# Kernel tuning notes

Measured on AMD Instinct MI355X. Metric: run time of the kernel, lower is better.

Reference implementation:

```python
import jax, jax.numpy as jnp
import numpy as np

B = 256        # number of trees
L0 = 4096      # leaves per tree
L1 = 256       # layer-1 nodes per tree
D = 128        # input_dim == hidden_dim
OUT = 32       # output classes
EPS = 1e-5
N0 = B * L0    # 1,048,576 total leaves
N1 = B * L1    # 65,536 layer-1 nodes
N2 = B         # one root per tree


def _bn(x, g, b):
    # training-mode BatchNorm1d: biased variance over the node axis
    m = jnp.mean(x, axis=0)
    v = jnp.mean((x - m) ** 2, axis=0)
    return g * (x - m) * jax.lax.rsqrt(v + EPS) + b


def _mlp(h, w1, b1, g, beta, w2, b2):
    # GIN-style 2-layer MLP: relu(bn(linear)) -> linear
    return jax.nn.relu(_bn(h @ w1 + b1, g, beta)) @ w2 + b2


def setup_inputs() -> dict:
    key = jax.random.key(0)
    ks = jax.random.split(key, 16)

    def lin(k, fin, fout):
        kw, kb = jax.random.split(k)
        s = 1.0 / np.sqrt(fin)
        return (jax.random.uniform(kw, (fin, fout), jnp.float32, -s, s),
                jax.random.uniform(kb, (fout,), jnp.float32, -s, s))

    x = jax.random.normal(ks[0], (N0, D), jnp.float32)
    # structured tree indices: contiguous children per parent, contiguous trees
    parent1 = jnp.arange(N0, dtype=jnp.int64) // (L0 // L1)   # leaf -> layer1 parent (global)
    parent2 = jnp.arange(N1, dtype=jnp.int64) // L1           # layer1 -> root (global)
    tree0 = jnp.arange(N0, dtype=jnp.int64) // L0             # leaf -> tree id
    tree1 = jnp.arange(N1, dtype=jnp.int64) // L1             # layer1 node -> tree id

    m1w1, m1b1 = lin(ks[1], D, D)
    m1w2, m1b2 = lin(ks[2], D, D)
    m2w1, m2b1 = lin(ks[3], D, D)
    m2w2, m2b2 = lin(ks[4], D, D)
    wp, bp = lin(ks[5], D + 2 * D, OUT)

    ones = jnp.ones((D,), jnp.float32)
    zeros = jnp.zeros((D,), jnp.float32)
    return {
        "x": x, "parent1": parent1, "parent2": parent2, "tree0": tree0, "tree1": tree1,
        "mlp1_w1": m1w1, "mlp1_b1": m1b1, "mlp1_g": ones, "mlp1_beta": zeros,
        "mlp1_w2": m1w2, "mlp1_b2": m1b2, "bn1_g": ones, "bn1_b": zeros,
        "mlp2_w1": m2w1, "mlp2_b1": m2b1, "mlp2_g": ones, "mlp2_beta": zeros,
        "mlp2_w2": m2w2, "mlp2_b2": m2b2, "bn2_g": ones, "bn2_b": zeros,
        "wp": wp, "bp": bp,
    }


def reference(x, parent1, parent2, tree0, tree1,
              mlp1_w1, mlp1_b1, mlp1_g, mlp1_beta, mlp1_w2, mlp1_b2, bn1_g, bn1_b,
              mlp2_w1, mlp2_b1, mlp2_g, mlp2_beta, mlp2_w2, mlp2_b2, bn2_g, bn2_b,
              wp, bp):
    # layer 1: sparse child-sum (spmm with all-ones tree adjacency == segment_sum)
    p1 = jax.ops.segment_sum(x, parent1, num_segments=N1)              # [N1, D]
    h1 = jax.nn.relu(_bn(_mlp(p1, mlp1_w1, mlp1_b1, mlp1_g, mlp1_beta, mlp1_w2, mlp1_b2), bn1_g, bn1_b))
    # layer 2 (roots)
    p2 = jax.ops.segment_sum(h1, parent2, num_segments=N2)             # [B, D]
    h2 = jax.nn.relu(_bn(_mlp(p2, mlp2_w1, mlp2_b1, mlp2_g, mlp2_beta, mlp2_w2, mlp2_b2), bn2_g, bn2_b))
    # tree sum-pooling of layers 0..depth-1; layer depth is already per-tree
    g0 = jax.ops.segment_sum(x, tree0, num_segments=B)                 # [B, D]
    g1 = jax.ops.segment_sum(h1, tree1, num_segments=B)                # [B, D]
    rep = jnp.concatenate([g0, g1, h2], axis=1)                        # [B, 3D]
    return jax.nn.softmax(rep @ wp + bp, axis=1)                       # [B, OUT]
```

## Files before the change

### kernel.cpp

```cpp
#include <hip/hip_runtime.h>
#include <math.h>

#define D      128
#define D4     32
#define NTREE  256
#define NL1    65536
#define EPSBN  1e-5f

#define SC_OFF 0L
#define SD_OFF 256L
#define G0_OFF 512L
#define P2_OFF 33280L
#define ZERO_CNT 66048
#define SA_OFF 66048L
#define SB_OFF 66304L
#define T2_OFF 66560L
#define PBA_OFF 99328L
#define PBB_OFF 361472L
#define T1_OFF 623616L
#define U_OFF  4817920L

#define FMA4(A_, S_, W_) { (A_).x = fmaf((S_),(W_).x,(A_).x); (A_).y = fmaf((S_),(W_).y,(A_).y); \
                           (A_).z = fmaf((S_),(W_).z,(A_).z); (A_).w = fmaf((S_),(W_).w,(A_).w); }
#define ADD4(A_, B_)     { (A_).x += (B_).x; (A_).y += (B_).y; (A_).z += (B_).z; (A_).w += (B_).w; }
#define SQ4(Q_, V_)      { (Q_).x = fmaf((V_).x,(V_).x,(Q_).x); (Q_).y = fmaf((V_).y,(V_).y,(Q_).y); \
                           (Q_).z = fmaf((V_).z,(V_).z,(Q_).z); (Q_).w = fmaf((V_).w,(V_).w,(Q_).w); }
#define F4Z              make_float4(0.f,0.f,0.f,0.f)

__device__ __forceinline__ unsigned short f2b(float f) {
    unsigned u = __float_as_uint(f);
    return (unsigned short)((u + 0x7FFFu + ((u >> 16) & 1u)) >> 16);
}
__device__ __forceinline__ float b2f(unsigned short h) {
    return __uint_as_float(((unsigned)h) << 16);
}

__global__ __launch_bounds__(256) void k_zero(float* __restrict__ ws) {
    int i = blockIdx.x * 256 + threadIdx.x;
    if (i < ZERO_CNT) ws[i] = 0.f;
}

__global__ __launch_bounds__(256) void k_fused1(const float* __restrict__ x,
        const float* __restrict__ w1, const float* __restrict__ b1,
        unsigned short* __restrict__ t1, float* __restrict__ g0,
        float* __restrict__ pbufA)
{
    __shared__ __align__(16) float tile[64][D];
    __shared__ __align__(16) float red[2][8][D];
    const int t = threadIdx.x, b = blockIdx.x;
    const int w  = t >> 6;
    const int ln = t & 63;
    const int lc = ln & 31;
    const float4* __restrict__ x4 = (const float4*)x;

    float4 gacc = F4Z;
    #pragma unroll
    for (int pp = 0; pp < 4; ++pp) {
        const int p0 = pp * 16 + w * 4;
        #pragma unroll
        for (int r = 0; r < 4; ++r) {
            const long prow = (long)b * 64 + p0 + r;
            const long base = prow * 512 + ln;
            float4 a = F4Z;
            #pragma unroll
            for (int j = 0; j < 8; ++j) {
                float4 v = x4[base + j * 64];
                ADD4(a, v)
            }
            float4 o;
            o.x = __shfl_xor(a.x, 32); o.y = __shfl_xor(a.y, 32);
            o.z = __shfl_xor(a.z, 32); o.w = __shfl_xor(a.w, 32);
            ADD4(a, o)
            if (ln < 32) {
                *(float4*)&tile[p0 + r][lc*4] = a;
                ADD4(gacc, a)
            }
        }
    }
    if (ln < 32) *(float4*)&red[0][w][lc*4] = gacc;
    __syncthreads();
    if (t < 32) {
        float4 G = F4Z;
        #pragma unroll
        for (int g = 0; g < 4; ++g) { float4 vg = *(const float4*)&red[0][g][t*4]; ADD4(G, vg) }
        const int tree = b >> 2;
        atomicAdd(&g0[tree*D + t*4+0], G.x); atomicAdd(&g0[tree*D + t*4+1], G.y);
        atomicAdd(&g0[tree*D + t*4+2], G.z); atomicAdd(&g0[tree*D + t*4+3], G.w);
    }

    const int tc = t & 31, rg = t >> 5;
    ushort4* __restrict__ tv = (ushort4*)t1;
    const long base = (long)b * 64;
    float4 acc[8];
    const float4 bb = ((const float4*)b1)[tc];
    #pragma unroll
    for (int r = 0; r < 8; ++r) acc[r] = bb;
    const float4* __restrict__ wv = (const float4*)w1;
    #pragma unroll 4
    for (int k4 = 0; k4 < 32; ++k4) {
        float4 wr0 = wv[(k4*4+0)*D4 + tc];
        float4 wr1 = wv[(k4*4+1)*D4 + tc];
        float4 wr2 = wv[(k4*4+2)*D4 + tc];
        float4 wr3 = wv[(k4*4+3)*D4 + tc];
        #pragma unroll
        for (int r = 0; r < 8; ++r) {
            float4 a4 = *(const float4*)&tile[rg*8 + r][k4*4];
            FMA4(acc[r], a4.x, wr0) FMA4(acc[r], a4.y, wr1)
            FMA4(acc[r], a4.z, wr2) FMA4(acc[r], a4.w, wr3)
        }
    }
    #pragma unroll
    for (int r = 0; r < 8; ++r) {
        ushort4 h;
        h.x = f2b(acc[r].x); h.y = f2b(acc[r].y);
        h.z = f2b(acc[r].z); h.w = f2b(acc[r].w);
        tv[(base + rg*8 + r) * D4 + tc] = h;
    }

    float4 s4 = F4Z, q4 = F4Z;
    #pragma unroll
    for (int r = 0; r < 8; ++r) { ADD4(s4, acc[r]) SQ4(q4, acc[r]) }
    __syncthreads();
    *(float4*)&red[0][rg][tc*4] = s4;
    *(float4*)&red[1][rg][tc*4] = q4;
    __syncthreads();
    if (t < 32) {
        float4 S = F4Z;
        #pragma unroll
        for (int g = 0; g < 8; ++g) { float4 vs = *(const float4*)&red[0][g][t*4]; ADD4(S, vs) }
        *(float4*)&pbufA[b*256 + t*4] = S;
    } else if (t < 64) {
        const int c = t - 32;
        float4 Q = F4Z;
        #pragma unroll
        for (int g = 0; g < 8; ++g) { float4 vq = *(const float4*)&red[1][g][c*4]; ADD4(Q, vq) }
        *(float4*)&pbufA[b*256 + 128 + c*4] = Q;
    }
}

__global__ __launch_bounds__(256) void k_statR(const float* __restrict__ pbuf,
                                               float* __restrict__ stats)
{
    __shared__ float red[8][32];
    const int t = threadIdx.x, b = blockIdx.x;
    const int c = b * 32 + (t & 31);
    const int g = t >> 5;
    float s = 0.f;
    #pragma unroll 8
    for (int r = g; r < 1024; r += 8) s += pbuf[r*256 + c];
    red[g][t & 31] = s;
    __syncthreads();
    if (t < 32) {
        float S = 0.f;
        #pragma unroll
        for (int gg = 0; gg < 8; ++gg) S += red[gg][t];
        stats[b*32 + t] = S;
    }
}

__global__ __launch_bounds__(256) void k_mm2(const unsigned short* __restrict__ t1,
        const float* __restrict__ w2, const float* __restrict__ b2,
        const float* __restrict__ mg, const float* __restrict__ mbe,
        const float* __restrict__ statsA, unsigned short* __restrict__ u,
        float* __restrict__ pbufB)
{
    __shared__ __align__(16) float tile[64][D];
    __shared__ __align__(16) float red[2][8][D];
    const int t = threadIdx.x, b = blockIdx.x;
    const int tc = t & 31, rg = t >> 5;
    const ushort4* __restrict__ tv = (const ushort4*)t1;
    ushort4* __restrict__ uv = (ushort4*)u;
    const long base = (long)b * 64;

    float4 scv, shv;
    {
        const float inv = 1.f / (float)NL1;
        #pragma unroll
        for (int i = 0; i < 4; ++i) {
            const int c = tc*4 + i;
            float m  = statsA[c] * inv;
            float vv = statsA[D + c] * inv - m * m;
            float rs = rsqrtf(vv + EPSBN);
            float sc = mg[c] * rs;
            ((float*)&scv)[i] = sc;
            ((float*)&shv)[i] = mbe[c] - m * sc;
        }
    }
    #pragma unroll
    for (int i = 0; i < 8; ++i) {
        const int row = i * 8 + rg;
        ushort4 hv = tv[(base + row) * D4 + tc];
        float4 v = make_float4(b2f(hv.x), b2f(hv.y), b2f(hv.z), b2f(hv.w));
        float4 y;
        y.x = fmaxf(fmaf(v.x, scv.x, shv.x), 0.f);
        y.y = fmaxf(fmaf(v.y, scv.y, shv.y), 0.f);
        y.z = fmaxf(fmaf(v.z, scv.z, shv.z), 0.f);
        y.w = fmaxf(fmaf(v.w, scv.w, shv.w), 0.f);
        *(float4*)&tile[row][tc*4] = y;
    }
    __syncthreads();

    float4 acc[8];
    const float4 bb = ((const float4*)b2)[tc];
    #pragma unroll
    for (int r = 0; r < 8; ++r) acc[r] = bb;
    const float4* __restrict__ wv = (const float4*)w2;
    #pragma unroll 4
    for (int k4 = 0; k4 < 32; ++k4) {
        float4 wr0 = wv[(k4*4+0)*D4 + tc];
        float4 wr1 = wv[(k4*4+1)*D4 + tc];
        float4 wr2 = wv[(k4*4+2)*D4 + tc];
        float4 wr3 = wv[(k4*4+3)*D4 + tc];
        #pragma unroll
        for (int r = 0; r < 8; ++r) {
            float4 a4 = *(const float4*)&tile[rg*8 + r][k4*4];
            FMA4(acc[r], a4.x, wr0) FMA4(acc[r], a4.y, wr1)
            FMA4(acc[r], a4.z, wr2) FMA4(acc[r], a4.w, wr3)
        }
    }
    #pragma unroll
    for (int r = 0; r < 8; ++r) {
        ushort4 h;
        h.x = f2b(acc[r].x); h.y = f2b(acc[r].y);
        h.z = f2b(acc[r].z); h.w = f2b(acc[r].w);
        uv[(base + rg*8 + r) * D4 + tc] = h;
    }

    float4 s4 = F4Z, q4 = F4Z;
    #pragma unroll
    for (int r = 0; r < 8; ++r) { ADD4(s4, acc[r]) SQ4(q4, acc[r]) }
    __syncthreads();
    *(float4*)&red[0][rg][tc*4] = s4;
    *(float4*)&red[1][rg][tc*4] = q4;
    __syncthreads();
    if (t < 32) {
        float4 S = F4Z;
        #pragma unroll
        for (int g = 0; g < 8; ++g) { float4 vs = *(const float4*)&red[0][g][t*4]; ADD4(S, vs) }
        *(float4*)&pbufB[b*256 + t*4] = S;
    } else if (t < 64) {
        const int c = t - 32;
        float4 Q = F4Z;
        #pragma unroll
        for (int g = 0; g < 8; ++g) { float4 vq = *(const float4*)&red[1][g][c*4]; ADD4(Q, vq) }
        *(float4*)&pbufB[b*256 + 128 + c*4] = Q;
    }
}

__global__ __launch_bounds__(256) void k_pool(const unsigned short* __restrict__ u,
        const float* __restrict__ bg, const float* __restrict__ bb_,
        const float* __restrict__ statsB, float* __restrict__ p2)
{
    __shared__ __align__(16) float red[8][D];
    const int t = threadIdx.x, b = blockIdx.x;
    const int tree = b >> 3, chunk = b & 7;
    const int tc = t & 31, rr = t >> 5;
    const ushort4* __restrict__ uv = (const ushort4*)u;

    float4 scv, shv;
    {
        const float inv = 1.f / (float)NL1;
        #pragma unroll
        for (int i = 0; i < 4; ++i) {
            const int c = tc*4 + i;
            float m  = statsB[c] * inv;
            float vv = statsB[D + c] * inv - m * m;
            float rs = rsqrtf(vv + EPSBN);
            float sc = bg[c] * rs;
            ((float*)&scv)[i] = sc;
            ((float*)&shv)[i] = bb_[c] - m * sc;
        }
    }
    const long rbase = (long)tree * 256 + chunk * 32;
    float4 ps = F4Z;
    #pragma unroll
    for (int i = 0; i < 4; ++i) {
        const int row = i * 8 + rr;
        ushort4 hv = uv[(rbase + row) * D4 + tc];
        float4 v = make_float4(b2f(hv.x), b2f(hv.y), b2f(hv.z), b2f(hv.w));
        ps.x += fmaxf(fmaf(v.x, scv.x, shv.x), 0.f);
        ps.y += fmaxf(fmaf(v.y, scv.y, shv.y), 0.f);
        ps.z += fmaxf(fmaf(v.z, scv.z, shv.z), 0.f);
        ps.w += fmaxf(fmaf(v.w, scv.w, shv.w), 0.f);
    }
    *(float4*)&red[rr][tc*4] = ps;
    __syncthreads();
    if (t < 32) {
        float4 S = F4Z;
        #pragma unroll
        for (int g = 0; g < 8; ++g) { float4 vs = *(const float4*)&red[g][t*4]; ADD4(S, vs) }
        atomicAdd(&p2[tree*D + t*4+0], S.x); atomicAdd(&p2[tree*D + t*4+1], S.y);
        atomicAdd(&p2[tree*D + t*4+2], S.z); atomicAdd(&p2[tree*D + t*4+3], S.w);
    }
}

__global__ __launch_bounds__(256) void k_root1(const float* __restrict__ p2,
        const float* __restrict__ w1, const float* __restrict__ b1,
        float* __restrict__ t2, float* __restrict__ statsC)
{
    __shared__ __align__(16) float ps[8][D];
    __shared__ __align__(16) float red[2][8][D];
    const int t = threadIdx.x, b = blockIdx.x;
    const int j4 = t & 31, rr = t >> 5;
    *(float4*)&ps[rr][j4*4] = ((const float4*)p2)[(b*8 + rr)*D4 + j4];
    __syncthreads();
    const int row = t >> 5, tc = t & 31;
    const float4* wv = (const float4*)w1;
    float4 acc = ((const float4*)b1)[tc];
    #pragma unroll 8
    for (int k4 = 0; k4 < 32; ++k4) {
        float4 a = *(const float4*)&ps[row][k4*4];
        float4 wr0 = wv[(k4*4+0)*D4 + tc];
        float4 wr1 = wv[(k4*4+1)*D4 + tc];
        float4 wr2 = wv[(k4*4+2)*D4 + tc];
        float4 wr3 = wv[(k4*4+3)*D4 + tc];
        FMA4(acc, a.x, wr0) FMA4(acc, a.y, wr1) FMA4(acc, a.z, wr2) FMA4(acc, a.w, wr3)
    }
    ((float4*)t2)[(b*8 + row)*D4 + tc] = acc;
    float4 q;
    q.x = acc.x*acc.x; q.y = acc.y*acc.y; q.z = acc.z*acc.z; q.w = acc.w*acc.w;
    *(float4*)&red[0][row][tc*4] = acc;
    *(float4*)&red[1][row][tc*4] = q;
    __syncthreads();
    if (t < D) {
        float S = 0.f, Q = 0.f;
        #pragma unroll
        for (int g = 0; g < 8; ++g) { S += red[0][g][t]; Q += red[1][g][t]; }
        atomicAdd(&statsC[t], S);
        atomicAdd(&statsC[D+t], Q);
    }
}

__global__ __launch_bounds__(256) void k_root2(float* __restrict__ t2,
        const float* __restrict__ mg, const float* __restrict__ mb,
        const float* __restrict__ statsC,
        const float* __restrict__ w2, const float* __restrict__ b2,
        float* __restrict__ statsD)
{
    __shared__ __align__(16) float ysr[8][D];
    __shared__ __align__(16) float red[2][8][D];
    __shared__ __align__(16) float scs[D], shs[D];
    const int t = threadIdx.x, b = blockIdx.x;
    if (t < D) {
        float m = statsC[t] * (1.f / 256.f);
        float v = statsC[D+t] * (1.f / 256.f) - m * m;
        float rs = rsqrtf(v + EPSBN);
        float sc = mg[t] * rs;
        scs[t] = sc;
        shs[t] = mb[t] - m * sc;
    }
    __syncthreads();
    const int j4 = t & 31, rr = t >> 5;
    {
        float4 uu = ((const float4*)t2)[(b*8 + rr)*D4 + j4];
        float4 sc4 = *(const float4*)&scs[j4*4];
        float4 sh4 = *(const float4*)&shs[j4*4];
        float4 y;
        y.x = fmaxf(fmaf(uu.x, sc4.x, sh4.x), 0.f);
        y.y = fmaxf(fmaf(uu.y, sc4.y, sh4.y), 0.f);
        y.z = fmaxf(fmaf(uu.z, sc4.z, sh4.z), 0.f);
        y.w = fmaxf(fmaf(uu.w, sc4.w, sh4.w), 0.f);
        *(float4*)&ysr[rr][j4*4] = y;
    }
    __syncthreads();
    const int row = t >> 5, tc = t & 31;
    const float4* wv = (const float4*)w2;
    float4 acc = ((const float4*)b2)[tc];
    #pragma unroll 8
    for (int k4 = 0; k4 < 32; ++k4) {
        float4 a = *(const float4*)&ysr[row][k4*4];
        float4 wr0 = wv[(k4*4+0)*D4 + tc];
        float4 wr1 = wv[(k4*4+1)*D4 + tc];
        float4 wr2 = wv[(k4*4+2)*D4 + tc];
        float4 wr3 = wv[(k4*4+3)*D4 + tc];
        FMA4(acc, a.x, wr0) FMA4(acc, a.y, wr1) FMA4(acc, a.z, wr2) FMA4(acc, a.w, wr3)
    }
    ((float4*)t2)[(b*8 + row)*D4 + tc] = acc;
    float4 q;
    q.x = acc.x*acc.x; q.y = acc.y*acc.y; q.z = acc.z*acc.z; q.w = acc.w*acc.w;
    *(float4*)&red[0][row][tc*4] = acc;
    *(float4*)&red[1][row][tc*4] = q;
    __syncthreads();
    if (t < D) {
        float S = 0.f, Q = 0.f;
        #pragma unroll
        for (int g = 0; g < 8; ++g) { S += red[0][g][t]; Q += red[1][g][t]; }
        atomicAdd(&statsD[t], S);
        atomicAdd(&statsD[D+t], Q);
    }
}

__global__ __launch_bounds__(128) void k_final(const float* __restrict__ u2,
        const float* __restrict__ statsD,
        const float* __restrict__ bg, const float* __restrict__ bb_,
        const float* __restrict__ g0, const float* __restrict__ p2,
        const float* __restrict__ wp, const float* __restrict__ bp,
        float* __restrict__ out)
{
    __shared__ __align__(16) float reps[3*D];
    const int t = threadIdx.x, tree = blockIdx.x;
    if (t < D) {
        float m = statsD[t] * (1.f / 256.f);
        float v = statsD[D+t] * (1.f / 256.f) - m * m;
        float rs = rsqrtf(v + EPSBN);
        float sc = bg[t] * rs;
        float sh = bb_[t] - m * sc;
        reps[2*D + t] = fmaxf(fmaf(u2[tree*D + t], sc, sh), 0.f);
        reps[t]       = g0[tree*D + t];
        reps[D + t]   = p2[tree*D + t];
    }
    __syncthreads();
    if (t < 32) {
        float acc = bp[t];
        #pragma unroll 8
        for (int j = 0; j < 3*D; ++j) acc = fmaf(reps[j], wp[j*32 + t], acc);
        float mx = acc;
        #pragma unroll
        for (int mk = 16; mk > 0; mk >>= 1) mx = fmaxf(mx, __shfl_xor(mx, mk));
        float e = expf(acc - mx);
        float s = e;
        #pragma unroll
        for (int mk = 16; mk > 0; mk >>= 1) s += __shfl_xor(s, mk);
        out[tree*32 + t] = e / s;
    }
}

extern "C" void kernel_launch(void* const* d_in, const int* in_sizes, int n_in,
                              void* d_out, int out_size, void* d_ws, size_t ws_size,
                              hipStream_t stream)
{
    const float* x    = (const float*)d_in[0];
    const float* m1w1 = (const float*)d_in[5];
    const float* m1b1 = (const float*)d_in[6];
    const float* m1g  = (const float*)d_in[7];
    const float* m1be = (const float*)d_in[8];
    const float* m1w2 = (const float*)d_in[9];
    const float* m1b2 = (const float*)d_in[10];
    const float* bn1g = (const float*)d_in[11];
    const float* bn1b = (const float*)d_in[12];
    const float* m2w1 = (const float*)d_in[13];
    const float* m2b1 = (const float*)d_in[14];
    const float* m2g  = (const float*)d_in[15];
    const float* m2be = (const float*)d_in[16];
    const float* m2w2 = (const float*)d_in[17];
    const float* m2b2 = (const float*)d_in[18];
    const float* bn2g = (const float*)d_in[19];
    const float* bn2b = (const float*)d_in[20];
    const float* wp   = (const float*)d_in[21];
    const float* bp   = (const float*)d_in[22];
    float* out = (float*)d_out;
    float* ws  = (float*)d_ws;

    float* sC  = ws + SC_OFF;
    float* sD  = ws + SD_OFF;
    float* g0  = ws + G0_OFF;
    float* p2  = ws + P2_OFF;
    float* sA  = ws + SA_OFF;
    float* sB  = ws + SB_OFF;
    float* t2  = ws + T2_OFF;
    float* pbA = ws + PBA_OFF;
    float* pbB = ws + PBB_OFF;
    unsigned short* t1 = (unsigned short*)(ws + T1_OFF);
    unsigned short* u  = (unsigned short*)(ws + U_OFF);

    hipLaunchKernelGGL(k_zero,   dim3(258),  dim3(256), 0, stream, ws);
    hipLaunchKernelGGL(k_fused1, dim3(1024), dim3(256), 0, stream, x, m1w1, m1b1, t1, g0, pbA);
    hipLaunchKernelGGL(k_statR,  dim3(8),    dim3(256), 0, stream, pbA, sA);
    hipLaunchKernelGGL(k_mm2,    dim3(1024), dim3(256), 0, stream, t1, m1w2, m1b2, m1g, m1be, sA, u, pbB);
    hipLaunchKernelGGL(k_statR,  dim3(8),    dim3(256), 0, stream, pbB, sB);
    hipLaunchKernelGGL(k_pool,   dim3(2048), dim3(256), 0, stream, u, bn1g, bn1b, sB, p2);
    hipLaunchKernelGGL(k_root1,  dim3(32),   dim3(256), 0, stream, p2, m2w1, m2b1, t2, sC);
    hipLaunchKernelGGL(k_root2,  dim3(32),   dim3(256), 0, stream, t2, m2g, m2be, sC, m2w2, m2b2, sD);
    hipLaunchKernelGGL(k_final,  dim3(256),  dim3(128), 0, stream, t2, sD, bn2g, bn2b, g0, p2, wp, bp, out);
}
```

Baseline: 236.7 us.

## Use bf16 MFMA for layer-1 MLP matmuls with pre-transposed bf16 weights

Measured after the change: 210.9 us (median of 2 runs). 10.9% less time.

```diff
diff --git a/kernel.cpp b/kernel.cpp
--- a/kernel.cpp
+++ b/kernel.cpp
@@ -17,15 +17,18 @@
 #define T2_OFF 66560L
 #define PBA_OFF 99328L
 #define PBB_OFF 361472L
-#define T1_OFF 623616L
-#define U_OFF  4817920L
+#define WT1_OFF 623616L
+#define WT2_OFF 631808L
+#define T1_OFF  640000L
+#define U_OFF   4834304L
 
 #define FMA4(A_, S_, W_) { (A_).x = fmaf((S_),(W_).x,(A_).x); (A_).y = fmaf((S_),(W_).y,(A_).y); \
                            (A_).z = fmaf((S_),(W_).z,(A_).z); (A_).w = fmaf((S_),(W_).w,(A_).w); }
 #define ADD4(A_, B_)     { (A_).x += (B_).x; (A_).y += (B_).y; (A_).z += (B_).z; (A_).w += (B_).w; }
-#define SQ4(Q_, V_)      { (Q_).x = fmaf((V_).x,(V_).x,(Q_).x); (Q_).y = fmaf((V_).y,(V_).y,(Q_).y); \
-                           (Q_).z = fmaf((V_).z,(V_).z,(Q_).z); (Q_).w = fmaf((V_).w,(V_).w,(Q_).w); }
 #define F4Z              make_float4(0.f,0.f,0.f,0.f)
+
+typedef short  bf16x8 __attribute__((ext_vector_type(8)));
+typedef float  f32x4  __attribute__((ext_vector_type(4)));
 
 __device__ __forceinline__ unsigned short f2b(float f) {
     unsigned u = __float_as_uint(f);
@@ -35,18 +38,32 @@
     return __uint_as_float(((unsigned)h) << 16);
 }
 
-__global__ __launch_bounds__(256) void k_zero(float* __restrict__ ws) {
-    int i = blockIdx.x * 256 + threadIdx.x;
-    if (i < ZERO_CNT) ws[i] = 0.f;
-}
-
-__global__ __launch_bounds__(256) void k_fused1(const float* __restrict__ x,
-        const float* __restrict__ w1, const float* __restrict__ b1,
+__global__ __launch_bounds__(256) void k_zp(float* __restrict__ ws,
+        const float* __restrict__ w1, const float* __restrict__ w2,
+        unsigned short* __restrict__ wT1, unsigned short* __restrict__ wT2)
+{
+    const int b = blockIdx.x, t = threadIdx.x;
+    if (b < 258) {
+        int i = b * 256 + t;
+        if (i < ZERO_CNT) ws[i] = 0.f;
+    } else {
+        int idx = (b - 258) * 256 + t;
+        int mat = idx >> 14;
+        int e   = idx & 16383;
+        int n = e >> 7, k = e & 127;
+        const float* wsrc = mat ? w2 : w1;
+        unsigned short* wd = mat ? wT2 : wT1;
+        wd[n*128 + k] = f2b(wsrc[k*128 + n]);
+    }
+}
+
+__global__ __launch_bounds__(256, 6) void k_fused1(const float* __restrict__ x,
+        const unsigned short* __restrict__ wT1, const float* __restrict__ b1,
         unsigned short* __restrict__ t1, float* __restrict__ g0,
         float* __restrict__ pbufA)
 {
-    __shared__ __align__(16) float tile[64][D];
-    __shared__ __align__(16) float red[2][8][D];
+    __shared__ __align__(16) unsigned short tileu[64][136];
+    __shared__ __align__(16) float g0red[4][D];
     const int t = threadIdx.x, b = blockIdx.x;
     const int w  = t >> 6;
     const int ln = t & 63;
@@ -63,78 +80,72 @@
             const long base = prow * 512 + ln;
             float4 a = F4Z;
             #pragma unroll
-            for (int j = 0; j < 8; ++j) {
-                float4 v = x4[base + j * 64];
-                ADD4(a, v)
-            }
+            for (int j = 0; j < 8; ++j) { float4 v = x4[base + j * 64]; ADD4(a, v) }
             float4 o;
             o.x = __shfl_xor(a.x, 32); o.y = __shfl_xor(a.y, 32);
             o.z = __shfl_xor(a.z, 32); o.w = __shfl_xor(a.w, 32);
             ADD4(a, o)
             if (ln < 32) {
-                *(float4*)&tile[p0 + r][lc*4] = a;
+                ushort4 h;
+                h.x = f2b(a.x); h.y = f2b(a.y); h.z = f2b(a.z); h.w = f2b(a.w);
+                *(ushort4*)&tileu[p0 + r][lc*4] = h;
                 ADD4(gacc, a)
             }
         }
     }
-    if (ln < 32) *(float4*)&red[0][w][lc*4] = gacc;
+    if (ln < 32) *(float4*)&g0red[w][lc*4] = gacc;
     __syncthreads();
     if (t < 32) {
         float4 G = F4Z;
         #pragma unroll
-        for (int g = 0; g < 4; ++g) { float4 vg = *(const float4*)&red[0][g][t*4]; ADD4(G, vg) }
+        for (int g = 0; g < 4; ++g) { float4 vg = *(const float4*)&g0red[g][t*4]; ADD4(G, vg) }
         const int tree = b >> 2;
         atomicAdd(&g0[tree*D + t*4+0], G.x); atomicAdd(&g0[tree*D + t*4+1], G.y);
         atomicAdd(&g0[tree*D + t*4+2], G.z); atomicAdd(&g0[tree*D + t*4+3], G.w);
     }
 
-    const int tc = t & 31, rg = t >> 5;
-    ushort4* __restrict__ tv = (ushort4*)t1;
-    const long base = (long)b * 64;
-    float4 acc[8];
-    const float4 bb = ((const float4*)b1)[tc];
-    #pragma unroll
-    for (int r = 0; r < 8; ++r) acc[r] = bb;
-    const float4* __restrict__ wv = (const float4*)w1;
-    #pragma unroll 4
-    for (int k4 = 0; k4 < 32; ++k4) {
-        float4 wr0 = wv[(k4*4+0)*D4 + tc];
-        float4 wr1 = wv[(k4*4+1)*D4 + tc];
-        float4 wr2 = wv[(k4*4+2)*D4 + tc];
-        float4 wr3 = wv[(k4*4+3)*D4 + tc];
-        #pragma unroll
-        for (int r = 0; r < 8; ++r) {
-            float4 a4 = *(const float4*)&tile[rg*8 + r][k4*4];
-            FMA4(acc[r], a4.x, wr0) FMA4(acc[r], a4.y, wr1)
-            FMA4(acc[r], a4.z, wr2) FMA4(acc[r], a4.w, wr3)
-        }
-    }
-    #pragma unroll
-    for (int r = 0; r < 8; ++r) {
-        ushort4 h;
-        h.x = f2b(acc[r].x); h.y = f2b(acc[r].y);
-        h.z = f2b(acc[r].z); h.w = f2b(acc[r].w);
-        tv[(base + rg*8 + r) * D4 + tc] = h;
-    }
-
-    float4 s4 = F4Z, q4 = F4Z;
-    #pragma unroll
-    for (int r = 0; r < 8; ++r) { ADD4(s4, acc[r]) SQ4(q4, acc[r]) }
-    __syncthreads();
-    *(float4*)&red[0][rg][tc*4] = s4;
-    *(float4*)&red[1][rg][tc*4] = q4;
-    __syncthreads();
-    if (t < 32) {
-        float4 S = F4Z;
-        #pragma unroll
-        for (int g = 0; g < 8; ++g) { float4 vs = *(const float4*)&red[0][g][t*4]; ADD4(S, vs) }
-        *(float4*)&pbufA[b*256 + t*4] = S;
-    } else if (t < 64) {
-        const int c = t - 32;
-        float4 Q = F4Z;
-        #pragma unroll
-        for (int g = 0; g < 8; ++g) { float4 vq = *(const float4*)&red[1][g][c*4]; ADD4(Q, vq) }
-        *(float4*)&pbufA[b*256 + 128 + c*4] = Q;
+    const int lq = ln >> 4;
+    const int lr = ln & 15;
+    bf16x8 av[4];
+    #pragma unroll
+    for (int ks = 0; ks < 4; ++ks)
+        av[ks] = *(const bf16x8*)&tileu[w*16 + lr][ks*32 + lq*8];
+    __syncthreads();
+
+    const long rowbase = (long)b * 64;
+    float sP[8], qP[8];
+    #pragma unroll
+    for (int cb = 0; cb < 8; ++cb) {
+        f32x4 acc = {0.f, 0.f, 0.f, 0.f};
+        #pragma unroll
+        for (int ks = 0; ks < 4; ++ks) {
+            bf16x8 bv = *(const bf16x8*)&wT1[(cb*16 + lr)*128 + ks*32 + lq*8];
+            acc = __builtin_amdgcn_mfma_f32_16x16x32_bf16(av[ks], bv, acc, 0, 0, 0);
+        }
+        const float bc = b1[cb*16 + lr];
+        float s = 0.f, q = 0.f;
+        #pragma unroll
+        for (int j = 0; j < 4; ++j) {
+            float v = acc[j] + bc;
+            t1[(rowbase + w*16 + lq*4 + j)*128 + cb*16 + lr] = f2b(v);
+            s += v; q = fmaf(v, v, q);
+        }
+        sP[cb] = s; qP[cb] = q;
+    }
+
+    float* sq = (float*)tileu;
+    #pragma unroll
+    for (int cb = 0; cb < 8; ++cb) {
+        sq[(w*4 + lq)*128 + cb*16 + lr]        = sP[cb];
+        sq[2048 + (w*4 + lq)*128 + cb*16 + lr] = qP[cb];
+    }
+    __syncthreads();
+    if (t < 128) {
+        float S = 0.f, Q = 0.f;
+        #pragma unroll
+        for (int r = 0; r < 16; ++r) { S += sq[r*128 + t]; Q += sq[2048 + r*128 + t]; }
+        pbufA[b*256 + t]       = S;
+        pbufA[b*256 + 128 + t] = Q;
     }
 }
 
@@ -158,18 +169,15 @@
     }
 }
 
-__global__ __launch_bounds__(256) void k_mm2(const unsigned short* __restrict__ t1,
-        const float* __restrict__ w2, const float* __restrict__ b2,
+__global__ __launch_bounds__(256, 6) void k_mm2(const unsigned short* __restrict__ t1,
+        const unsigned short* __restrict__ wT2, const float* __restrict__ b2,
         const float* __restrict__ mg, const float* __restrict__ mbe,
         const float* __restrict__ statsA, unsigned short* __restrict__ u,
         float* __restrict__ pbufB)
 {
-    __shared__ __align__(16) float tile[64][D];
-    __shared__ __align__(16) float red[2][8][D];
+    __shared__ __align__(16) unsigned short tileu[64][136];
     const int t = threadIdx.x, b = blockIdx.x;
     const int tc = t & 31, rg = t >> 5;
-    const ushort4* __restrict__ tv = (const ushort4*)t1;
-    ushort4* __restrict__ uv = (ushort4*)u;
     const long base = (long)b * 64;
 
     float4 scv, shv;
@@ -189,61 +197,60 @@
     #pragma unroll
     for (int i = 0; i < 8; ++i) {
         const int row = i * 8 + rg;
-        ushort4 hv = tv[(base + row) * D4 + tc];
-        float4 v = make_float4(b2f(hv.x), b2f(hv.y), b2f(hv.z), b2f(hv.w));
+        ushort4 hv = *(const ushort4*)&t1[(base + row)*128 + tc*4];
         float4 y;
-        y.x = fmaxf(fmaf(v.x, scv.x, shv.x), 0.f);
-        y.y = fmaxf(fmaf(v.y, scv.y, shv.y), 0.f);
-        y.z = fmaxf(fmaf(v.z, scv.z, shv.z), 0.f);
-        y.w = fmaxf(fmaf(v.w, scv.w, shv.w), 0.f);
-        *(float4*)&tile[row][tc*4] = y;
-    }
-    __syncthreads();
-
-    float4 acc[8];
-    const float4 bb = ((const float4*)b2)[tc];
-    #pragma unroll
-    for (int r = 0; r < 8; ++r) acc[r] = bb;
-    const float4* __restrict__ wv = (const float4*)w2;
-    #pragma unroll 4
-    for (int k4 = 0; k4 < 32; ++k4) {
-        float4 wr0 = wv[(k4*4+0)*D4 + tc];
-        float4 wr1 = wv[(k4*4+1)*D4 + tc];
-        float4 wr2 = wv[(k4*4+2)*D4 + tc];
-        float4 wr3 = wv[(k4*4+3)*D4 + tc];
-        #pragma unroll
-        for (int r = 0; r < 8; ++r) {
-            float4 a4 = *(const float4*)&tile[rg*8 + r][k4*4];
-            FMA4(acc[r], a4.x, wr0) FMA4(acc[r], a4.y, wr1)
-            FMA4(acc[r], a4.z, wr2) FMA4(acc[r], a4.w, wr3)
-        }
-    }
-    #pragma unroll
-    for (int r = 0; r < 8; ++r) {
+        y.x = fmaxf(fmaf(b2f(hv.x), scv.x, shv.x), 0.f);
+        y.y = fmaxf(fmaf(b2f(hv.y), scv.y, shv.y), 0.f);
+        y.z = fmaxf(fmaf(b2f(hv.z), scv.z, shv.z), 0.f);
+        y.w = fmaxf(fmaf(b2f(hv.w), scv.w, shv.w), 0.f);
         ushort4 h;
-        h.x = f2b(acc[r].x); h.y = f2b(acc[r].y);
-        h.z = f2b(acc[r].z); h.w = f2b(acc[r].w);
-        uv[(base + rg*8 + r) * D4 + tc] = h;
-    }
-
-    float4 s4 = F4Z, q4 = F4Z;
-    #pragma unroll
-    for (int r = 0; r < 8; ++r) { ADD4(s4, acc[r]) SQ4(q4, acc[r]) }
-    __syncthreads();
-    *(float4*)&red[0][rg][tc*4] = s4;
-    *(float4*)&red[1][rg][tc*4] = q4;
-    __syncthreads();
-    if (t < 32) {
-        float4 S = F4Z;
-        #pragma unroll
-        for (int g = 0; g < 8; ++g) { float4 vs = *(const float4*)&red[0][g][t*4]; ADD4(S, vs) }
-        *(float4*)&pbufB[b*256 + t*4] = S;
-    } else if (t < 64) {
-        const int c = t - 32;
-        float4 Q = F4Z;
-        #pragma unroll
-        for (int g = 0; g < 8; ++g) { float4 vq = *(const float4*)&red[1][g][c*4]; ADD4(Q, vq) }
-        *(float4*)&pbufB[b*256 + 128 + c*4] = Q;
+        h.x = f2b(y.x); h.y = f2b(y.y); h.z = f2b(y.z); h.w = f2b(y.w);
+        *(ushort4*)&tileu[row][tc*4] = h;
+    }
+    __syncthreads();
+
+    const int w  = t >> 6;
+    const int ln = t & 63;
+    const int lq = ln >> 4, lr = ln & 15;
+    bf16x8 av[4];
+    #pragma unroll
+    for (int ks = 0; ks < 4; ++ks)
+        av[ks] = *(const bf16x8*)&tileu[w*16 + lr][ks*32 + lq*8];
+    __syncthreads();
+
+    float sP[8], qP[8];
+    #pragma unroll
+    for (int cb = 0; cb < 8; ++cb) {
+        f32x4 acc = {0.f, 0.f, 0.f, 0.f};
+        #pragma unroll
+        for (int ks = 0; ks < 4; ++ks) {
+            bf16x8 bv = *(const bf16x8*)&wT2[(cb*16 + lr)*128 + ks*32 + lq*8];
+            acc = __builtin_amdgcn_mfma_f32_16x16x32_bf16(av[ks], bv, acc, 0, 0, 0);
+        }
+        const float bc = b2[cb*16 + lr];
+        float s = 0.f, q = 0.f;
+        #pragma unroll
+        for (int j = 0; j < 4; ++j) {
+            float v = acc[j] + bc;
+            u[(base + w*16 + lq*4 + j)*128 + cb*16 + lr] = f2b(v);
+            s += v; q = fmaf(v, v, q);
+        }
+        sP[cb] = s; qP[cb] = q;
+    }
+
+    float* sq = (float*)tileu;
+    #pragma unroll
+    for (int cb = 0; cb < 8; ++cb) {
+        sq[(w*4 + lq)*128 + cb*16 + lr]        = sP[cb];
+        sq[2048 + (w*4 + lq)*128 + cb*16 + lr] = qP[cb];
+    }
+    __syncthreads();
+    if (t < 128) {
+        float S = 0.f, Q = 0.f;
+        #pragma unroll
+        for (int r = 0; r < 16; ++r) { S += sq[r*128 + t]; Q += sq[2048 + r*128 + t]; }
+        pbufB[b*256 + t]       = S;
+        pbufB[b*256 + 128 + t] = Q;
     }
 }
 
@@ -460,13 +467,15 @@
     float* t2  = ws + T2_OFF;
     float* pbA = ws + PBA_OFF;
     float* pbB = ws + PBB_OFF;
-    unsigned short* t1 = (unsigned short*)(ws + T1_OFF);
-    unsigned short* u  = (unsigned short*)(ws + U_OFF);
-
-    hipLaunchKernelGGL(k_zero,   dim3(258),  dim3(256), 0, stream, ws);
-    hipLaunchKernelGGL(k_fused1, dim3(1024), dim3(256), 0, stream, x, m1w1, m1b1, t1, g0, pbA);
+    unsigned short* wT1 = (unsigned short*)(ws + WT1_OFF);
+    unsigned short* wT2 = (unsigned short*)(ws + WT2_OFF);
+    unsigned short* t1  = (unsigned short*)(ws + T1_OFF);
+    unsigned short* u   = (unsigned short*)(ws + U_OFF);
+
+    hipLaunchKernelGGL(k_zp,     dim3(386),  dim3(256), 0, stream, ws, m1w1, m1w2, wT1, wT2);
+    hipLaunchKernelGGL(k_fused1, dim3(1024), dim3(256), 0, stream, x, wT1, m1b1, t1, g0, pbA);
     hipLaunchKernelGGL(k_statR,  dim3(8),    dim3(256), 0, stream, pbA, sA);
-    hipLaunchKernelGGL(k_mm2,    dim3(1024), dim3(256), 0, stream, t1, m1w2, m1b2, m1g, m1be, sA, u, pbB);
+    hipLaunchKernelGGL(k_mm2,    dim3(1024), dim3(256), 0, stream, t1, wT2, m1b2, m1g, m1be, sA, u, pbB);
     hipLaunchKernelGGL(k_statR,  dim3(8),    dim3(256), 0, stream, pbB, sB);
     hipLaunchKernelGGL(k_pool,   dim3(2048), dim3(256), 0, stream, u, bn1g, bn1b, sB, p2);
     hipLaunchKernelGGL(k_root1,  dim3(32),   dim3(256), 0, stream, p2, m2w1, m2b1, t2, sC);
```
